# Kernel optimization log

Measured on AMD Instinct MI355X. Metric: run time of the kernel, lower is better.

Reference implementation:

```python
import jax, jax.numpy as jnp
import numpy as np

B, T, D = 4, 4096, 1024

def setup_inputs() -> dict:
    key = jax.random.key(0)
    kx, kq, kk, kv = jax.random.split(key, 4)
    return {
        "x": jax.random.normal(kx, (B, T, D), dtype=jnp.float32),
        "w_q": jax.random.normal(kq, (D, D), dtype=jnp.float32),
        "w_k": jax.random.normal(kk, (D, D), dtype=jnp.float32),
        "w_v": jax.random.normal(kv, (D, D), dtype=jnp.float32),
    }

def reference(x, w_q, w_k, w_v):
    # Projections: (B,T,D) @ (D,D) -> (B,T,D)
    q = jnp.einsum('btk,kd->btd', x, w_q)
    k = jnp.einsum('btk,kd->btd', x, w_k)
    v = jnp.einsum('btk,kd->btd', x, w_v)
    d = x.shape[-1]
    # Faithful to source: gamma = 1/sqrt(1/d) = sqrt(d) (multiplies, not divides)
    gamma = jnp.sqrt(jnp.asarray(d, dtype=x.dtype))
    a = jnp.einsum('bqd,bkd->bqk', q, k) * gamma  # (B,T,T), no softmax
    y = jnp.einsum('bqt,btd->bqd', a, v)          # (B,T,D)
    return y
```

## Files before the change

kernel.cpp:

```cpp
#include <hip/hip_runtime.h>
#include <hip/hip_bf16.h>


typedef __attribute__((ext_vector_type(8))) short bf16x8;
typedef __attribute__((ext_vector_type(4))) float f32x4;

__device__ __forceinline__ unsigned short bf16bits(float f) {
    union { __hip_bfloat16 b; unsigned short s; } r;
    r.b = __float2bfloat16(f);
    return r.s;
}

__device__ __forceinline__ void gload16(const void* g, void* l) {
    __builtin_amdgcn_global_load_lds((__attribute__((address_space(1))) void*)g,
                                     (__attribute__((address_space(3))) void*)l,
                                     16, 0, 0);
}

template<int TM, int TN, int MODE, bool OUT_F32>
__global__ __launch_bounds__(256)
void gemm_nt(const __hip_bfloat16* __restrict__ Ap, const __hip_bfloat16* __restrict__ Bp,
             void* __restrict__ Cp, int N, int Kc, int ldA, int ldB,
             long sA, long sB, long sC, int nb, float scale)
{
    constexpr int FM = TM / 32;
    constexpr int FN = TN / 32;

    __shared__ __hip_bfloat16 At[2][TM][32];
    __shared__ __hip_bfloat16 Bt[2][TN][32];

    const int gx = (int)gridDim.x, gy = (int)gridDim.y, gz = (int)gridDim.z;
    int slice, tile;
    if (MODE == 0) {
        slice = blockIdx.z;
        int wg = blockIdx.y * gx + blockIdx.x;
        const int cpx = (gx * gy) >> 3;
        tile = (wg & 7) * cpx + (wg >> 3);
    } else {
        const int h = ((int)blockIdx.z * gy + (int)blockIdx.y) * gx + (int)blockIdx.x;
        const int xcd = h & 7, k = h >> 3;
        if (MODE == 1) {
            const int SL = gz >> 3;
            slice = xcd + 8 * (k % SL);
            tile  = k / SL;
        } else {
            slice = xcd % gz;
            tile  = (xcd / gz) * ((gx * gy * gz) >> 3) + k;
        }
    }
    const int batch = slice % nb;
    const int kc    = slice / nb;
    const int n0 = (tile % gx) * TN;
    const int m0 = (tile / gx) * TM;

    const int tid  = threadIdx.x;
    const int lane = tid & 63;
    const int wave = tid >> 6;
    const int wm = (wave & 1) * (TM / 2);
    const int wn = (wave >> 1) * (TN / 2);
    const int l16 = lane & 15;
    const int lq  = lane >> 4;

    const int aoff = wave * (TM * 8) + lane * 8;
    const int boff = wave * (TN * 8) + lane * 8;
    const int arow = aoff >> 5, brow = boff >> 5;
    const int acs = (((aoff >> 3) & 3) ^ ((aoff >> 6) & 3)) << 3;
    const int bcs = (((boff >> 3) & 3) ^ ((boff >> 6) & 3)) << 3;
    const int sc = (lq ^ ((l16 >> 1) & 3)) << 3;

    const __hip_bfloat16* Ab = Ap + (size_t)batch * sA + (size_t)kc * Kc;
    const __hip_bfloat16* Bb = Bp + (size_t)batch * sB + (size_t)kc * Kc;

    auto stage = [&](int buf, int k0) {
        #pragma unroll
        for (int i = 0; i < TM / 64; ++i)
            gload16(Ab + (size_t)(m0 + arow + i * 16) * ldA + k0 + acs,
                    &At[buf][0][0] + aoff + i * 512);
        #pragma unroll
        for (int i = 0; i < TN / 64; ++i)
            gload16(Bb + (size_t)(n0 + brow + i * 16) * ldB + k0 + bcs,
                    &Bt[buf][0][0] + boff + i * 512);
    };

    f32x4 acc[FM][FN];
    #pragma unroll
    for (int i = 0; i < FM; ++i)
        #pragma unroll
        for (int j = 0; j < FN; ++j)
            acc[i][j] = (f32x4){0.f, 0.f, 0.f, 0.f};

    stage(0, 0);
    __syncthreads();

    const int nt = Kc >> 5;
    for (int t = 0; t < nt; ++t) {
        const int cur = t & 1;
        if (t + 1 < nt) stage(cur ^ 1, (t + 1) << 5);

        bf16x8 av[FM], bv[FN];
        #pragma unroll
        for (int i = 0; i < FM; ++i)
            av[i] = *(const bf16x8*)&At[cur][wm + i * 16 + l16][sc];
        #pragma unroll
        for (int j = 0; j < FN; ++j)
            bv[j] = *(const bf16x8*)&Bt[cur][wn + j * 16 + l16][sc];
        #pragma unroll
        for (int i = 0; i < FM; ++i)
            #pragma unroll
            for (int j = 0; j < FN; ++j)
                acc[i][j] = __builtin_amdgcn_mfma_f32_16x16x32_bf16(av[i], bv[j], acc[i][j], 0, 0, 0);
        __syncthreads();
    }

    float* Cf = (float*)Cp;
    __hip_bfloat16* Ch = (__hip_bfloat16*)Cp;
    const size_t cb0 = (size_t)slice * sC;
    #pragma unroll
    for (int i = 0; i < FM; ++i) {
        #pragma unroll
        for (int j = 0; j < FN; ++j) {
            const int row0 = m0 + wm + i * 16 + lq * 4;
            const int col  = n0 + wn + j * 16 + l16;
            #pragma unroll
            for (int r = 0; r < 4; ++r) {
                float v = acc[i][j][r] * scale;
                size_t idx = cb0 + (size_t)(row0 + r) * N + col;
                if (OUT_F32) Cf[idx] = v;
                else         Ch[idx] = __float2bfloat16(v);
            }
        }
    }
}

__global__ __launch_bounds__(256)
void reduce_kchunks(const unsigned short* __restrict__ part,
                    unsigned short* __restrict__ out)
{
    const size_t l = ((size_t)blockIdx.x * 256 + threadIdx.x) * 8;
    const size_t DD4 = (size_t)4 << 20;
    union { unsigned short h[8]; uint4 u; } a, b, o;
    a.u = *(const uint4*)(part + l);
    b.u = *(const uint4*)(part + l + DD4);
    #pragma unroll
    for (int j = 0; j < 8; ++j) {
        union { float f; unsigned int u; } fa, fb;
        fa.u = (unsigned int)a.h[j] << 16;
        fb.u = (unsigned int)b.h[j] << 16;
        o.h[j] = bf16bits(fa.f + fb.f);
    }
    *(uint4*)(out + l) = o.u;
}

#define TP 64
__global__ __launch_bounds__(256)
void transpose_cast(const float* __restrict__ in, __hip_bfloat16* __restrict__ out,
                    __hip_bfloat16* __restrict__ straight, int nsb,
                    int R, int C, long inStride, long outStride)
{
    __shared__ __hip_bfloat16 t2[TP][TP + 4];
    const int b  = blockIdx.z;
    const int r0 = blockIdx.x * TP;
    const int c0 = blockIdx.y * TP;
    const float* inb = in + (size_t)b * inStride;
    __hip_bfloat16* outb = out + (size_t)b * outStride;
    __hip_bfloat16* stb  = straight + (size_t)b * inStride;
    const int t  = threadIdx.x;
    const int rr = t >> 4;
    const int c4 = (t & 15) * 4;
    #pragma unroll
    for (int p = 0; p < 4; ++p) {
        const int row = p * 16 + rr;
        float4 f = *(const float4*)&inb[(size_t)(r0 + row) * C + c0 + c4];
        union { __hip_bfloat16 h[4]; uint2 u; } s;
        s.h[0] = __float2bfloat16(f.x); s.h[1] = __float2bfloat16(f.y);
        s.h[2] = __float2bfloat16(f.z); s.h[3] = __float2bfloat16(f.w);
        t2[c4 + 0][row] = s.h[0];
        t2[c4 + 1][row] = s.h[1];
        t2[c4 + 2][row] = s.h[2];
        t2[c4 + 3][row] = s.h[3];
        if (b < nsb)
            *(uint2*)&stb[(size_t)(r0 + row) * C + c0 + c4] = s.u;
    }
    __syncthreads();
    #pragma unroll
    for (int p = 0; p < 4; ++p) {
        const int crow = p * 16 + rr;
        union { __hip_bfloat16 h[4]; uint2 u; } o;
        #pragma unroll
        for (int j = 0; j < 4; ++j) o.h[j] = t2[crow][c4 + j];
        *(uint2*)&outb[(size_t)(c0 + crow) * R + r0 + c4] = o.u;
    }
}

__global__ __launch_bounds__(256)
void cast_f32_bf16(const float* __restrict__ in, __hip_bfloat16* __restrict__ out, int n)
{
    const int i = (blockIdx.x * 256 + threadIdx.x) << 2;
    if (i >= n) return;
    float4 f = *(const float4*)(in + i);
    union { __hip_bfloat16 h[4]; uint2 u; } t;
    t.h[0] = __float2bfloat16(f.x); t.h[1] = __float2bfloat16(f.y);
    t.h[2] = __float2bfloat16(f.z); t.h[3] = __float2bfloat16(f.w);
    *(uint2*)(out + i) = t.u;
}

extern "C" void kernel_launch(void* const* d_in, const int* in_sizes, int n_in,
                              void* d_out, int out_size, void* d_ws, size_t ws_size,
                              hipStream_t stream)
{
    const int Bz = 4, T = 4096, D = 1024;
    const float gamma = 32.0f;

    const float* x  = (const float*)d_in[0];
    const float* wq = (const float*)d_in[1];
    const float* wk = (const float*)d_in[2];
    const float* wv = (const float*)d_in[3];
    float* y = (float*)d_out;

    unsigned char* p = (unsigned char*)d_ws;
    const size_t DD = (size_t)D * D;
    __hip_bfloat16* Gb  = (__hip_bfloat16*)p; p += Bz * DD * 2;
    __hip_bfloat16* Hb  = (__hip_bfloat16*)p; p += Bz * DD * 2;
    __hip_bfloat16* PTb = (__hip_bfloat16*)p; p += Bz * DD * 2;
    __hip_bfloat16* wqb = (__hip_bfloat16*)p; p += DD * 2;
    __hip_bfloat16* wkb = (__hip_bfloat16*)p; p += DD * 2;
    __hip_bfloat16* wvT = (__hip_bfloat16*)p; p += DD * 2;
    __hip_bfloat16* C0b = (__hip_bfloat16*)p; p += DD * 2;
    __hip_bfloat16* Gpart = Hb;
    __hip_bfloat16* xb23  = Gb;

    __hip_bfloat16* xbT  = (__hip_bfloat16*)d_out;
    __hip_bfloat16* xb01 = (__hip_bfloat16*)((unsigned char*)d_out + ((size_t)32 << 20));

    dim3 blk(256);

    cast_f32_bf16<<<dim3((int)(DD / 1024)), blk, 0, stream>>>(wq, wqb, (int)DD);
    cast_f32_bf16<<<dim3((int)(DD / 1024)), blk, 0, stream>>>(wk, wkb, (int)DD);
    transpose_cast<<<dim3(D / TP, D / TP, 1), blk, 0, stream>>>(
        wv, wvT, wvT, 0, D, D, 0, 0);
    transpose_cast<<<dim3(T / TP, D / TP, Bz), blk, 0, stream>>>(
        x, xbT, xb01, 2, T, D, (long)T * D, (long)D * T);

    gemm_nt<64, 128, 0, false><<<dim3(D / 128, D / 64, 1), blk, 0, stream>>>(
        wqb, wkb, C0b, D, D, D, D, 0, 0, 0, 1, 1.0f);
    gemm_nt<128, 128, 1, false><<<dim3(D / 128, D / 128, 2 * Bz), blk, 0, stream>>>(
        xbT, xbT, Gpart, D, T / 2, T, T, (long)D * T, (long)D * T, (long)DD, Bz, 1.0f);
    reduce_kchunks<<<dim3((int)(Bz * DD / 2048)), blk, 0, stream>>>(
        (const unsigned short*)Gpart, (unsigned short*)Gb);
    gemm_nt<64, 128, 2, false><<<dim3(D / 128, D / 64, Bz), blk, 0, stream>>>(
        C0b, Gb, Hb, D, D, D, D, 0, (long)DD, (long)DD, Bz, 1.0f);
    gemm_nt<64, 128, 2, false><<<dim3(D / 128, D / 64, Bz), blk, 0, stream>>>(
        wvT, Hb, PTb, D, D, D, D, 0, (long)DD, (long)DD, Bz, gamma);

    cast_f32_bf16<<<dim3((int)(2 * (size_t)T * D / 1024)), blk, 0, stream>>>(
        x + (size_t)2 * T * D, xb23, (int)(2 * (size_t)T * D));

    gemm_nt<128, 128, 2, true><<<dim3(D / 128, T / 128, 2), blk, 0, stream>>>(
        xb01, PTb, y, D, D, D, D, (long)T * D, (long)DD, (long)T * D, 2, 1.0f);
    gemm_nt<128, 128, 2, true><<<dim3(D / 128, T / 128, 2), blk, 0, stream>>>(
        xb23, PTb + 2 * DD, y + (size_t)2 * T * D, D, D, D, D,
        (long)T * D, (long)DD, (long)T * D, 2, 1.0f);
}
```

Measured before the change: 293.6 us.

## Add 512-thread 256x128 triple-buffered GEMM kernel for Gram and output GEMMs

```diff
diff --git a/kernel.cpp b/kernel.cpp
--- a/kernel.cpp
+++ b/kernel.cpp
@@ -15,6 +15,113 @@
     __builtin_amdgcn_global_load_lds((__attribute__((address_space(1))) void*)g,
                                      (__attribute__((address_space(3))) void*)l,
                                      16, 0, 0);
+}
+
+template<int MODE, bool OUT_F32>
+__global__ __launch_bounds__(512, 2)
+void gemm8(const __hip_bfloat16* __restrict__ Ap, const __hip_bfloat16* __restrict__ Bp,
+           void* __restrict__ Cp, int N, int Kc, int ldA, int ldB,
+           long sA, long sB, long sC, int nb, int tnc, float scale)
+{
+    constexpr int BM = 256, BN = 128, BK = 64;
+    __shared__ __hip_bfloat16 lds[3][(BM + BN) * BK];
+
+    const int h = blockIdx.x;
+    int slice, tile;
+    if (MODE == 1) { slice = h & 7; tile = h >> 3; }
+    else {
+        const int xcd = h & 7;
+        slice = xcd % nb;
+        tile  = (xcd / nb) * ((int)gridDim.x >> 3) + (h >> 3);
+    }
+    const int batch = slice % nb, kc = slice / nb;
+    const int n0 = (tile % tnc) * BN;
+    const int m0 = (tile / tnc) * BM;
+
+    const int tid  = threadIdx.x;
+    const int lane = tid & 63;
+    const int w    = tid >> 6;
+    const int wm = (w >> 1) * 64, wn = (w & 1) * 64;
+    const int l16 = lane & 15, lq = lane >> 4;
+
+    const int srow = lane >> 3;
+    const int scol = ((lane & 7) ^ srow) << 3;
+    const int soff = w * 512 + lane * 8;
+
+    const __hip_bfloat16* Ab = Ap + (size_t)batch * sA + (size_t)kc * Kc;
+    const __hip_bfloat16* Bb = Bp + (size_t)batch * sB + (size_t)kc * Kc;
+
+    const int nt = Kc >> 6;
+    auto stage = [&](int buf, int t) {
+        const int k0 = (t < nt ? t : nt - 1) << 6;
+        __hip_bfloat16* L = &lds[buf][0];
+        #pragma unroll
+        for (int i = 0; i < 4; ++i)
+            gload16(Ab + (size_t)(m0 + i * 64 + w * 8 + srow) * ldA + k0 + scol,
+                    L + i * 4096 + soff);
+        #pragma unroll
+        for (int i = 0; i < 2; ++i)
+            gload16(Bb + (size_t)(n0 + i * 64 + w * 8 + srow) * ldB + k0 + scol,
+                    L + BM * BK + i * 4096 + soff);
+    };
+
+    f32x4 acc[4][4];
+    #pragma unroll
+    for (int i = 0; i < 4; ++i)
+        #pragma unroll
+        for (int j = 0; j < 4; ++j)
+            acc[i][j] = (f32x4){0.f, 0.f, 0.f, 0.f};
+
+    stage(0, 0);
+    stage(1, 1);
+
+    for (int t = 0; t < nt; ++t) {
+        asm volatile("s_waitcnt vmcnt(6)" ::: "memory");
+        __builtin_amdgcn_s_barrier();
+        asm volatile("" ::: "memory");
+        stage((t + 2) % 3, t + 2);
+
+        const __hip_bfloat16* LA = &lds[t % 3][0];
+        const __hip_bfloat16* LB = LA + BM * BK;
+        #pragma unroll
+        for (int kk = 0; kk < 2; ++kk) {
+            const int sc = ((kk * 4 + lq) ^ (l16 & 7)) << 3;
+            bf16x8 av[4], bv[4];
+            #pragma unroll
+            for (int i = 0; i < 4; ++i)
+                av[i] = *(const bf16x8*)&LA[(wm + i * 16 + l16) * BK + sc];
+            #pragma unroll
+            for (int j = 0; j < 4; ++j)
+                bv[j] = *(const bf16x8*)&LB[(wn + j * 16 + l16) * BK + sc];
+            __builtin_amdgcn_s_setprio(1);
+            #pragma unroll
+            for (int i = 0; i < 4; ++i)
+                #pragma unroll
+                for (int j = 0; j < 4; ++j)
+                    acc[i][j] = __builtin_amdgcn_mfma_f32_16x16x32_bf16(av[i], bv[j], acc[i][j], 0, 0, 0);
+            __builtin_amdgcn_s_setprio(0);
+        }
+    }
+    asm volatile("s_waitcnt vmcnt(0)" ::: "memory");
+
+    float* Cf = (float*)Cp;
+    __hip_bfloat16* Ch = (__hip_bfloat16*)Cp;
+    const size_t cb0 = (size_t)slice * sC;
+    #pragma unroll
+    for (int i = 0; i < 4; ++i) {
+        #pragma unroll
+        for (int j = 0; j < 4; ++j) {
+            const int row0 = m0 + wm + i * 16 + lq * 4;
+            const int col  = n0 + wn + j * 16 + l16;
+            #pragma unroll
+            for (int r = 0; r < 4; ++r) {
+                float v = acc[i][j][r] * scale;
+                size_t idx = cb0 + (size_t)(row0 + r) * N + col;
+                if (OUT_F32) Cf[idx] = v;
+                else         Ch[idx] = __float2bfloat16(v);
+            }
+        }
+    }
 }
 
 template<int TM, int TN, int MODE, bool OUT_F32>
@@ -243,8 +350,8 @@
 
     gemm_nt<64, 128, 0, false><<<dim3(D / 128, D / 64, 1), blk, 0, stream>>>(
         wqb, wkb, C0b, D, D, D, D, 0, 0, 0, 1, 1.0f);
-    gemm_nt<128, 128, 1, false><<<dim3(D / 128, D / 128, 2 * Bz), blk, 0, stream>>>(
-        xbT, xbT, Gpart, D, T / 2, T, T, (long)D * T, (long)D * T, (long)DD, Bz, 1.0f);
+    gemm8<1, false><<<dim3(256), dim3(512), 0, stream>>>(
+        xbT, xbT, Gpart, D, T / 2, T, T, (long)D * T, (long)D * T, (long)DD, Bz, 8, 1.0f);
     reduce_kchunks<<<dim3((int)(Bz * DD / 2048)), blk, 0, stream>>>(
         (const unsigned short*)Gpart, (unsigned short*)Gb);
     gemm_nt<64, 128, 2, false><<<dim3(D / 128, D / 64, Bz), blk, 0, stream>>>(
@@ -255,9 +362,9 @@
     cast_f32_bf16<<<dim3((int)(2 * (size_t)T * D / 1024)), blk, 0, stream>>>(
         x + (size_t)2 * T * D, xb23, (int)(2 * (size_t)T * D));
 
-    gemm_nt<128, 128, 2, true><<<dim3(D / 128, T / 128, 2), blk, 0, stream>>>(
-        xb01, PTb, y, D, D, D, D, (long)T * D, (long)DD, (long)T * D, 2, 1.0f);
-    gemm_nt<128, 128, 2, true><<<dim3(D / 128, T / 128, 2), blk, 0, stream>>>(
+    gemm8<2, true><<<dim3(256), dim3(512), 0, stream>>>(
+        xb01, PTb, y, D, D, D, D, (long)T * D, (long)DD, (long)T * D, 2, 8, 1.0f);
+    gemm8<2, true><<<dim3(256), dim3(512), 0, stream>>>(
         xb23, PTb + 2 * DD, y + (size_t)2 * T * D, D, D, D, D,
-        (long)T * D, (long)DD, (long)T * D, 2, 1.0f);
-}
+        (long)T * D, (long)DD, (long)T * D, 2, 8, 1.0f);
+}
```

Result: faster. 275.6 us (-6.2%).
